# Optimization experiments

Measured on AMD Instinct MI355X. Metric: run time of the kernel, lower is better.

Reference implementation:

```python
import jax, jax.numpy as jnp
import numpy as np

B, S, CTXD, QD, ATTD = 32, 4096, 512, 512, 256

def setup_inputs() -> dict:
    key = jax.random.key(0)
    ks = jax.random.split(key, 7)
    qry = jax.random.normal(ks[0], (B, QD), dtype=jnp.float32)
    ctx = jax.random.normal(ks[1], (B, S, CTXD), dtype=jnp.float32)
    ctx_mask = jax.random.randint(ks[2], (B, S), 0, 2, dtype=jnp.int32)
    # ensure no all-zero row (would make softmax NaN)
    ctx_mask = ctx_mask.at[:, 0].set(1)
    sc = 1.0 / np.sqrt(CTXD + QD)
    W = jax.random.uniform(ks[3], (CTXD + QD, ATTD), jnp.float32, -sc, sc)
    b = jax.random.uniform(ks[4], (ATTD,), jnp.float32, -sc, sc)
    sc2 = 1.0 / np.sqrt(ATTD)
    w2 = jax.random.uniform(ks[5], (ATTD, 1), jnp.float32, -sc2, sc2)
    b2 = jax.random.uniform(ks[6], (1,), jnp.float32, -sc2, sc2)
    return {"qry": qry, "ctx": ctx, "ctx_mask": ctx_mask, "W": W, "b": b, "w2": w2, "b2": b2}

def reference(qry, ctx, ctx_mask, W, b, w2, b2):
    # cat([ctx, qry_rep]) @ W == ctx @ W_ctx + qry @ W_qry ; avoids the [B,S,ctxdim+qdim] concat
    W_ctx, W_qry = W[:CTXD], W[CTXD:]
    h = jnp.einsum('bsc,ca->bsa', ctx, W_ctx) + (qry @ W_qry)[:, None, :] + b  # [B,S,ATTD]
    y = jnp.tanh(h)
    scores = jnp.einsum('bsa,a->bs', y, w2[:, 0]) + b2[0]  # [B,S]
    scores = scores + jnp.log(ctx_mask.astype(jnp.float32))
    alphas = jax.nn.softmax(scores, axis=-1)  # [B,S]
    summary = jnp.einsum('bsc,bs->bc', ctx, alphas)  # [B,CTXD]
    return (alphas, summary, scores)
```

## Files before the change

kernel.cpp:

```cpp
#include <hip/hip_runtime.h>
#include <math.h>

#define B_ 32
#define S_ 4096
#define CTXD_ 512
#define QD_ 512
#define ATTD_ 256

#define KT 64
#define RT 64

#define MASKED_SCORE (-1e30f)

typedef __attribute__((ext_vector_type(8))) short bf16x8;
typedef __attribute__((ext_vector_type(4))) float f32x4;

__device__ __forceinline__ unsigned short f2bf(float f) {
    unsigned u = __float_as_uint(f);
    u += 0x7fff + ((u >> 16) & 1);
    return (unsigned short)(u >> 16);
}
__device__ __forceinline__ unsigned pk2(float lo, float hi) {
    return (unsigned)f2bf(lo) | ((unsigned)f2bf(hi) << 16);
}

__device__ __forceinline__ float fast_tanh(float x) {
    float xc = fminf(fmaxf(x, -15.f), 15.f);
    float t = __expf(2.f * xc);
    return (t - 1.f) / (t + 1.f);
}

__global__ __launch_bounds__(256) void wt_kernel(const float* __restrict__ W,
                                                 unsigned short* __restrict__ Wt) {
    __shared__ unsigned short tile[64][266];
    const int t = threadIdx.x;
    const int kk = blockIdx.x * 64;
    #pragma unroll
    for (int i = 0; i < 16; ++i) {
        const int r = i * 4 + (t >> 6);
        float4 v = ((const float4*)(W + (size_t)(kk + r) * ATTD_))[t & 63];
        unsigned short* tr = &tile[r][(t & 63) * 4];
        tr[0] = f2bf(v.x); tr[1] = f2bf(v.y);
        tr[2] = f2bf(v.z); tr[3] = f2bf(v.w);
    }
    __syncthreads();
    const int l8 = (t & 7) * 8;
    #pragma unroll
    for (int p = 0; p < 8; ++p) {
        const int n = p * 32 + (t >> 3);
        uint4 o;
        o.x = (unsigned)tile[l8 + 0][n] | ((unsigned)tile[l8 + 1][n] << 16);
        o.y = (unsigned)tile[l8 + 2][n] | ((unsigned)tile[l8 + 3][n] << 16);
        o.z = (unsigned)tile[l8 + 4][n] | ((unsigned)tile[l8 + 5][n] << 16);
        o.w = (unsigned)tile[l8 + 6][n] | ((unsigned)tile[l8 + 7][n] << 16);
        *(uint4*)(Wt + (size_t)n * CTXD_ + kk + l8) = o;
    }
}

__global__ __launch_bounds__(256) void qh_kernel(const float* __restrict__ qry,
                                                 const float* __restrict__ W,
                                                 const float* __restrict__ bias,
                                                 float* __restrict__ qh) {
    __shared__ float q[QD_];
    const int b = blockIdx.x, t = threadIdx.x;
    for (int i = t; i < QD_; i += 256) q[i] = qry[b * QD_ + i];
    __syncthreads();
    float acc = bias[t];
    const float* Wq = W + (size_t)CTXD_ * ATTD_ + t;
    #pragma unroll 8
    for (int k = 0; k < QD_; ++k) acc += q[k] * Wq[(size_t)k * ATTD_];
    qh[b * ATTD_ + t] = acc;
}

__global__ __launch_bounds__(256, 3) void scores_kernel(
    const float* __restrict__ ctx, const unsigned short* __restrict__ Wt,
    const float* __restrict__ qh, const float* __restrict__ w2,
    const float* __restrict__ b2, const int* __restrict__ mask,
    float* __restrict__ scores) {
    __shared__ unsigned char lds_a[RT * 144];
    __shared__ unsigned char lds_b[ATTD_ * 144];
    const int t = threadIdx.x;
    const int b = blockIdx.y;
    const int s0 = blockIdx.x * RT;
    const int tx = t & 63;
    const int w = t >> 6;
    const int wm = w & 1;
    const int wn = w >> 1;
    const int frow = tx & 15;
    const int fq = tx >> 4;

    f32x4 c00, c01, c02, c03, c04, c05, c06, c07;
    f32x4 c10, c11, c12, c13, c14, c15, c16, c17;
    c00 = c01 = c02 = c03 = c04 = c05 = c06 = c07 = (f32x4)0.f;
    c10 = c11 = c12 = c13 = c14 = c15 = c16 = c17 = (f32x4)0.f;

    const float* ctxb = ctx + ((size_t)b * S_ + s0) * CTXD_;
    const int arow = t >> 2;
    const int akq = t & 3;
    const int bn = t;

    const unsigned char* aBase = lds_a + (wm * 32 + frow) * 144 + fq * 16;
    const unsigned char* bBase = lds_b + (wn * 128 + frow) * 144 + fq * 16;

    const float* sA = ctxb + (size_t)arow * CTXD_ + akq * 16;
    float4 fa0 = ((const float4*)sA)[0];
    float4 fa1 = ((const float4*)sA)[1];
    float4 fa2 = ((const float4*)sA)[2];
    float4 fa3 = ((const float4*)sA)[3];
    const uint4* sB = (const uint4*)(Wt + (size_t)bn * CTXD_);
    uint4 pb0 = sB[0], pb1 = sB[1], pb2 = sB[2], pb3 = sB[3];
    uint4 pb4 = sB[4], pb5 = sB[5], pb6 = sB[6], pb7 = sB[7];

#define MM1(ni, ks, C0, C1)                                                  \
    {                                                                        \
        bf16x8 bf = *(const bf16x8*)(bBase + (ni) * (16 * 144) + (ks) * 64); \
        C0 = __builtin_amdgcn_mfma_f32_16x16x32_bf16(a0, bf, C0, 0, 0, 0);   \
        C1 = __builtin_amdgcn_mfma_f32_16x16x32_bf16(a1, bf, C1, 0, 0, 0);   \
    }
#define MMK(ks)                                                              \
    {                                                                        \
        bf16x8 a0 = *(const bf16x8*)(aBase + (ks) * 64);                     \
        bf16x8 a1 = *(const bf16x8*)(aBase + 16 * 144 + (ks) * 64);          \
        MM1(0, ks, c00, c10) MM1(1, ks, c01, c11) MM1(2, ks, c02, c12)       \
        MM1(3, ks, c03, c13) MM1(4, ks, c04, c14) MM1(5, ks, c05, c15)       \
        MM1(6, ks, c06, c16) MM1(7, ks, c07, c17)                            \
    }

    #pragma unroll 1
    for (int k0 = 0; k0 < CTXD_; k0 += KT) {
        __syncthreads();
        {
            uint4 p;
            p.x = pk2(fa0.x, fa0.y); p.y = pk2(fa0.z, fa0.w);
            p.z = pk2(fa1.x, fa1.y); p.w = pk2(fa1.z, fa1.w);
            *(uint4*)(lds_a + arow * 144 + akq * 32) = p;
            p.x = pk2(fa2.x, fa2.y); p.y = pk2(fa2.z, fa2.w);
            p.z = pk2(fa3.x, fa3.y); p.w = pk2(fa3.z, fa3.w);
            *(uint4*)(lds_a + arow * 144 + akq * 32 + 16) = p;
            uint4* bw = (uint4*)(lds_b + bn * 144);
            bw[0] = pb0; bw[1] = pb1; bw[2] = pb2; bw[3] = pb3;
            bw[4] = pb4; bw[5] = pb5; bw[6] = pb6; bw[7] = pb7;
        }
        __syncthreads();
        if (k0 + KT < CTXD_) {
            const float* sA2 = ctxb + (size_t)arow * CTXD_ + (k0 + KT) + akq * 16;
            fa0 = ((const float4*)sA2)[0];
            fa1 = ((const float4*)sA2)[1];
            fa2 = ((const float4*)sA2)[2];
            fa3 = ((const float4*)sA2)[3];
            const uint4* sB2 = (const uint4*)(Wt + (size_t)bn * CTXD_ + (k0 + KT));
            pb0 = sB2[0]; pb1 = sB2[1]; pb2 = sB2[2]; pb3 = sB2[3];
            pb4 = sB2[4]; pb5 = sB2[5]; pb6 = sB2[6]; pb7 = sB2[7];
        }
        MMK(0)
        MMK(1)
    }
#undef MMK
#undef MM1

    const float* qhb = qh + b * ATTD_ + wn * 128;
    const float* w2b = w2 + wn * 128;
    float p00 = 0.f, p01 = 0.f, p02 = 0.f, p03 = 0.f;
    float p10 = 0.f, p11 = 0.f, p12 = 0.f, p13 = 0.f;
#define EPI(ni, C0, C1)                                                      \
    {                                                                        \
        float qv = qhb[(ni) * 16 + frow];                                    \
        float wv = w2b[(ni) * 16 + frow];                                    \
        p00 += fast_tanh(C0[0] + qv) * wv;                                   \
        p01 += fast_tanh(C0[1] + qv) * wv;                                   \
        p02 += fast_tanh(C0[2] + qv) * wv;                                   \
        p03 += fast_tanh(C0[3] + qv) * wv;                                   \
        p10 += fast_tanh(C1[0] + qv) * wv;                                   \
        p11 += fast_tanh(C1[1] + qv) * wv;                                   \
        p12 += fast_tanh(C1[2] + qv) * wv;                                   \
        p13 += fast_tanh(C1[3] + qv) * wv;                                   \
    }
    EPI(0, c00, c10) EPI(1, c01, c11) EPI(2, c02, c12) EPI(3, c03, c13)
    EPI(4, c04, c14) EPI(5, c05, c15) EPI(6, c06, c16) EPI(7, c07, c17)
#undef EPI
    #pragma unroll
    for (int off = 1; off <= 8; off <<= 1) {
        p00 += __shfl_xor(p00, off, 64);
        p01 += __shfl_xor(p01, off, 64);
        p02 += __shfl_xor(p02, off, 64);
        p03 += __shfl_xor(p03, off, 64);
        p10 += __shfl_xor(p10, off, 64);
        p11 += __shfl_xor(p11, off, 64);
        p12 += __shfl_xor(p12, off, 64);
        p13 += __shfl_xor(p13, off, 64);
    }
    float* sred = (float*)lds_a;
    __syncthreads();
    if (frow == 0) {
        const int base = wn * 64 + wm * 32 + fq * 4;
        sred[base + 0] = p00; sred[base + 1] = p01;
        sred[base + 2] = p02; sred[base + 3] = p03;
        sred[base + 16 + 0] = p10; sred[base + 16 + 1] = p11;
        sred[base + 16 + 2] = p12; sred[base + 16 + 3] = p13;
    }
    __syncthreads();
    if (t < 64) {
        const int s = s0 + t;
        float sc = sred[t] + sred[64 + t] + b2[0];
        if (mask[b * S_ + s] == 0) sc = MASKED_SCORE;
        scores[b * S_ + s] = sc;
    }
}

__global__ __launch_bounds__(256) void softstat_kernel(
    const float* __restrict__ scores, float* __restrict__ stats) {
    const int b = blockIdx.x, t = threadIdx.x;
    __shared__ float red[8];
    float v[16];
    float m = -INFINITY;
    #pragma unroll
    for (int i = 0; i < 16; ++i) {
        v[i] = scores[b * S_ + t + i * 256];
        m = fmaxf(m, v[i]);
    }
    #pragma unroll
    for (int off = 1; off <= 32; off <<= 1) m = fmaxf(m, __shfl_xor(m, off, 64));
    if ((t & 63) == 0) red[t >> 6] = m;
    __syncthreads();
    m = fmaxf(fmaxf(red[0], red[1]), fmaxf(red[2], red[3]));
    float sum = 0.f;
    #pragma unroll
    for (int i = 0; i < 16; ++i) sum += expf(v[i] - m);
    #pragma unroll
    for (int off = 1; off <= 32; off <<= 1) sum += __shfl_xor(sum, off, 64);
    if ((t & 63) == 0) red[4 + (t >> 6)] = sum;
    __syncthreads();
    if (t == 0) {
        sum = red[4] + red[5] + red[6] + red[7];
        stats[2 * b] = m;
        stats[2 * b + 1] = 1.0f / sum;
    }
}

__global__ __launch_bounds__(256) void summary_part_kernel(
    const float* __restrict__ ctx, const float* __restrict__ scores,
    const float* __restrict__ stats, float* __restrict__ alphas,
    float* __restrict__ part, int nch, int cs) {
    const int b = blockIdx.y, ch = blockIdx.x, t = threadIdx.x;
    const int col = t & 63;
    const int q = t >> 6;
    const int s0 = ch * cs;
    const float m = stats[2 * b];
    const float invl = stats[2 * b + 1];
    const float* sp = scores + b * S_ + s0;
    for (int s = t; s < cs; s += 256)
        alphas[b * S_ + s0 + s] = expf(sp[s] - m) * invl;
    float4 alo = make_float4(0.f, 0.f, 0.f, 0.f);
    float4 ahi = make_float4(0.f, 0.f, 0.f, 0.f);
    const float* cp = ctx + ((size_t)b * S_ + s0) * CTXD_;
    #pragma unroll 4
    for (int s = q; s < cs; s += 4) {
        float al = expf(sp[s] - m) * invl;
        const float4* row = (const float4*)(cp + (size_t)s * CTXD_);
        float4 v0 = row[col];
        float4 v1 = row[col + 64];
        alo.x += v0.x * al; alo.y += v0.y * al;
        alo.z += v0.z * al; alo.w += v0.w * al;
        ahi.x += v1.x * al; ahi.y += v1.y * al;
        ahi.z += v1.z * al; ahi.w += v1.w * al;
    }
    __shared__ float4 buf[4][128];
    buf[q][col] = alo;
    buf[q][col + 64] = ahi;
    __syncthreads();
    if (t < 128) {
        float4 a0 = buf[0][t], a1 = buf[1][t], a2 = buf[2][t], a3 = buf[3][t];
        float4 r;
        r.x = a0.x + a1.x + a2.x + a3.x;
        r.y = a0.y + a1.y + a2.y + a3.y;
        r.z = a0.z + a1.z + a2.z + a3.z;
        r.w = a0.w + a1.w + a2.w + a3.w;
        ((float4*)(part + ((size_t)(b * nch + ch)) * CTXD_))[t] = r;
    }
}

__global__ __launch_bounds__(256) void summary_reduce_kernel(
    const float* __restrict__ part, float* __restrict__ summary, int nch) {
    const int b = blockIdx.x, t = threadIdx.x;
    for (int c = t; c < CTXD_; c += 256) {
        float s = 0.f;
        for (int ch = 0; ch < nch; ++ch)
            s += part[((size_t)(b * nch + ch)) * CTXD_ + c];
        summary[b * CTXD_ + c] = s;
    }
}

extern "C" void kernel_launch(void* const* d_in, const int* in_sizes, int n_in,
                              void* d_out, int out_size, void* d_ws,
                              size_t ws_size, hipStream_t stream) {
    const float* qry = (const float*)d_in[0];
    const float* ctx = (const float*)d_in[1];
    const int* mask = (const int*)d_in[2];
    const float* W = (const float*)d_in[3];
    const float* bias = (const float*)d_in[4];
    const float* w2 = (const float*)d_in[5];
    const float* b2 = (const float*)d_in[6];

    float* out = (float*)d_out;
    float* alphas = out;
    float* summary = out + B_ * S_;
    float* scores = out + B_ * S_ + B_ * CTXD_;

    unsigned short* Wt = (unsigned short*)d_ws;
    float* qh = (float*)((char*)d_ws + (size_t)ATTD_ * CTXD_ * 2);
    float* stats = qh + B_ * ATTD_;
    float* part = stats + 2 * B_;
    const size_t fixed_bytes =
        (size_t)ATTD_ * CTXD_ * 2 + (size_t)B_ * ATTD_ * 4 + 2 * B_ * 4;

    int nch = 64;
    while (nch > 1 && fixed_bytes + (size_t)B_ * nch * CTXD_ * 4 > ws_size)
        nch >>= 1;
    const int cs = S_ / nch;

    wt_kernel<<<8, 256, 0, stream>>>(W, Wt);
    qh_kernel<<<B_, 256, 0, stream>>>(qry, W, bias, qh);
    scores_kernel<<<dim3(S_ / RT, B_), 256, 0, stream>>>(ctx, Wt, qh, w2, b2,
                                                         mask, scores);
    softstat_kernel<<<B_, 256, 0, stream>>>(scores, stats);
    summary_part_kernel<<<dim3(nch, B_), 256, 0, stream>>>(ctx, scores, stats,
                                                           alphas, part, nch, cs);
    summary_reduce_kernel<<<B_, 256, 0, stream>>>(part, summary, nch);
}
```

Baseline: 520.2 us.

## Fuse softmax partial stats and weighted ctx sum into scores kernel

The scores kernel now computes per-chunk max and exp-sum, and accumulates the exp-weighted ctx rows for its tile into partial summaries. A new combine kernel rescales chunk partials by global max (online softmax), producing summary and alphas. This avoids a second full pass over ctx from global memory and drops two launches. The scores kernel gets extra epilogue work and the workspace-size fallback is removed.

```diff
diff --git a/kernel.cpp b/kernel.cpp
--- a/kernel.cpp
+++ b/kernel.cpp
@@ -9,6 +9,7 @@
 
 #define KT 64
 #define RT 64
+#define NCH (S_ / RT)
 
 #define MASKED_SCORE (-1e30f)
 
@@ -76,12 +77,14 @@
     const float* __restrict__ ctx, const unsigned short* __restrict__ Wt,
     const float* __restrict__ qh, const float* __restrict__ w2,
     const float* __restrict__ b2, const int* __restrict__ mask,
-    float* __restrict__ scores) {
+    float* __restrict__ scores, float* __restrict__ mstat,
+    float* __restrict__ lstat, float* __restrict__ part) {
     __shared__ unsigned char lds_a[RT * 144];
     __shared__ unsigned char lds_b[ATTD_ * 144];
     const int t = threadIdx.x;
     const int b = blockIdx.y;
-    const int s0 = blockIdx.x * RT;
+    const int ch = blockIdx.x;
+    const int s0 = ch * RT;
     const int tx = t & 63;
     const int w = t >> 6;
     const int wm = w & 1;
@@ -199,64 +202,37 @@
         sred[base + 16 + 2] = p12; sred[base + 16 + 3] = p13;
     }
     __syncthreads();
+    float* wl = (float*)lds_b;
     if (t < 64) {
         const int s = s0 + t;
         float sc = sred[t] + sred[64 + t] + b2[0];
-        if (mask[b * S_ + s] == 0) sc = MASKED_SCORE;
+        const bool msk = (mask[b * S_ + s] == 0);
+        if (msk) sc = MASKED_SCORE;
         scores[b * S_ + s] = sc;
-    }
-}
-
-__global__ __launch_bounds__(256) void softstat_kernel(
-    const float* __restrict__ scores, float* __restrict__ stats) {
-    const int b = blockIdx.x, t = threadIdx.x;
-    __shared__ float red[8];
-    float v[16];
-    float m = -INFINITY;
-    #pragma unroll
-    for (int i = 0; i < 16; ++i) {
-        v[i] = scores[b * S_ + t + i * 256];
-        m = fmaxf(m, v[i]);
-    }
-    #pragma unroll
-    for (int off = 1; off <= 32; off <<= 1) m = fmaxf(m, __shfl_xor(m, off, 64));
-    if ((t & 63) == 0) red[t >> 6] = m;
-    __syncthreads();
-    m = fmaxf(fmaxf(red[0], red[1]), fmaxf(red[2], red[3]));
-    float sum = 0.f;
-    #pragma unroll
-    for (int i = 0; i < 16; ++i) sum += expf(v[i] - m);
-    #pragma unroll
-    for (int off = 1; off <= 32; off <<= 1) sum += __shfl_xor(sum, off, 64);
-    if ((t & 63) == 0) red[4 + (t >> 6)] = sum;
-    __syncthreads();
-    if (t == 0) {
-        sum = red[4] + red[5] + red[6] + red[7];
-        stats[2 * b] = m;
-        stats[2 * b + 1] = 1.0f / sum;
-    }
-}
-
-__global__ __launch_bounds__(256) void summary_part_kernel(
-    const float* __restrict__ ctx, const float* __restrict__ scores,
-    const float* __restrict__ stats, float* __restrict__ alphas,
-    float* __restrict__ part, int nch, int cs) {
-    const int b = blockIdx.y, ch = blockIdx.x, t = threadIdx.x;
+        float mloc = sc;
+        #pragma unroll
+        for (int off = 1; off < 64; off <<= 1)
+            mloc = fmaxf(mloc, __shfl_xor(mloc, off, 64));
+        const float ws = msk ? 0.f : __expf(sc - mloc);
+        float lloc = ws;
+        #pragma unroll
+        for (int off = 1; off < 64; off <<= 1)
+            lloc += __shfl_xor(lloc, off, 64);
+        if (t == 0) {
+            mstat[b * NCH + ch] = mloc;
+            lstat[b * NCH + ch] = lloc;
+        }
+        wl[t] = ws;
+    }
+    __syncthreads();
     const int col = t & 63;
     const int q = t >> 6;
-    const int s0 = ch * cs;
-    const float m = stats[2 * b];
-    const float invl = stats[2 * b + 1];
-    const float* sp = scores + b * S_ + s0;
-    for (int s = t; s < cs; s += 256)
-        alphas[b * S_ + s0 + s] = expf(sp[s] - m) * invl;
     float4 alo = make_float4(0.f, 0.f, 0.f, 0.f);
     float4 ahi = make_float4(0.f, 0.f, 0.f, 0.f);
-    const float* cp = ctx + ((size_t)b * S_ + s0) * CTXD_;
     #pragma unroll 4
-    for (int s = q; s < cs; s += 4) {
-        float al = expf(sp[s] - m) * invl;
-        const float4* row = (const float4*)(cp + (size_t)s * CTXD_);
+    for (int s = q; s < RT; s += 4) {
+        const float al = wl[s];
+        const float4* row = (const float4*)(ctxb + (size_t)s * CTXD_);
         float4 v0 = row[col];
         float4 v1 = row[col + 64];
         alo.x += v0.x * al; alo.y += v0.y * al;
@@ -264,30 +240,64 @@
         ahi.x += v1.x * al; ahi.y += v1.y * al;
         ahi.z += v1.z * al; ahi.w += v1.w * al;
     }
-    __shared__ float4 buf[4][128];
-    buf[q][col] = alo;
-    buf[q][col + 64] = ahi;
+    float4* buf = (float4*)(lds_b + 1024);
+    buf[q * 128 + col] = alo;
+    buf[q * 128 + col + 64] = ahi;
     __syncthreads();
     if (t < 128) {
-        float4 a0 = buf[0][t], a1 = buf[1][t], a2 = buf[2][t], a3 = buf[3][t];
+        float4 a0 = buf[t], a1 = buf[128 + t], a2 = buf[256 + t], a3 = buf[384 + t];
         float4 r;
         r.x = a0.x + a1.x + a2.x + a3.x;
         r.y = a0.y + a1.y + a2.y + a3.y;
         r.z = a0.z + a1.z + a2.z + a3.z;
         r.w = a0.w + a1.w + a2.w + a3.w;
-        ((float4*)(part + ((size_t)(b * nch + ch)) * CTXD_))[t] = r;
-    }
-}
-
-__global__ __launch_bounds__(256) void summary_reduce_kernel(
-    const float* __restrict__ part, float* __restrict__ summary, int nch) {
+        ((float4*)(part + ((size_t)(b * NCH + ch)) * CTXD_))[t] = r;
+    }
+}
+
+__global__ __launch_bounds__(256) void combine_kernel(
+    const float* __restrict__ mstat, const float* __restrict__ lstat,
+    const float* __restrict__ part, const float* __restrict__ scores,
+    float* __restrict__ alphas, float* __restrict__ summary) {
     const int b = blockIdx.x, t = threadIdx.x;
-    for (int c = t; c < CTXD_; c += 256) {
-        float s = 0.f;
-        for (int ch = 0; ch < nch; ++ch)
-            s += part[((size_t)(b * nch + ch)) * CTXD_ + c];
-        summary[b * CTXD_ + c] = s;
-    }
+    __shared__ float e[NCH];
+    __shared__ float gstat[2];
+    if (t < NCH) {
+        const float mi = mstat[b * NCH + t];
+        const float li = lstat[b * NCH + t];
+        float m = mi;
+        #pragma unroll
+        for (int off = 1; off < 64; off <<= 1)
+            m = fmaxf(m, __shfl_xor(m, off, 64));
+        const float ei = __expf(mi - m);
+        float l = ei * li;
+        #pragma unroll
+        for (int off = 1; off < 64; off <<= 1)
+            l += __shfl_xor(l, off, 64);
+        e[t] = ei;
+        if (t == 0) { gstat[0] = m; gstat[1] = 1.0f / l; }
+    }
+    __syncthreads();
+    const float m = gstat[0], il = gstat[1];
+    const int c4 = t & 127, h = t >> 7;
+    float4 acc = make_float4(0.f, 0.f, 0.f, 0.f);
+    for (int chv = h; chv < NCH; chv += 2) {
+        const float ei = e[chv];
+        float4 v = ((const float4*)(part + ((size_t)(b * NCH + chv)) * CTXD_))[c4];
+        acc.x += ei * v.x; acc.y += ei * v.y;
+        acc.z += ei * v.z; acc.w += ei * v.w;
+    }
+    __shared__ float4 buf[128];
+    if (h == 1) buf[c4] = acc;
+    __syncthreads();
+    if (h == 0) {
+        float4 o = buf[c4];
+        acc.x = (acc.x + o.x) * il; acc.y = (acc.y + o.y) * il;
+        acc.z = (acc.z + o.z) * il; acc.w = (acc.w + o.w) * il;
+        ((float4*)(summary + (size_t)b * CTXD_))[c4] = acc;
+    }
+    for (int s = t; s < S_; s += 256)
+        alphas[b * S_ + s] = __expf(scores[b * S_ + s] - m) * il;
 }
 
 extern "C" void kernel_launch(void* const* d_in, const int* in_sizes, int n_in,
@@ -308,22 +318,14 @@
 
     unsigned short* Wt = (unsigned short*)d_ws;
     float* qh = (float*)((char*)d_ws + (size_t)ATTD_ * CTXD_ * 2);
-    float* stats = qh + B_ * ATTD_;
-    float* part = stats + 2 * B_;
-    const size_t fixed_bytes =
-        (size_t)ATTD_ * CTXD_ * 2 + (size_t)B_ * ATTD_ * 4 + 2 * B_ * 4;
-
-    int nch = 64;
-    while (nch > 1 && fixed_bytes + (size_t)B_ * nch * CTXD_ * 4 > ws_size)
-        nch >>= 1;
-    const int cs = S_ / nch;
+    float* mstat = qh + B_ * ATTD_;
+    float* lstat = mstat + B_ * NCH;
+    float* part = lstat + B_ * NCH;
 
     wt_kernel<<<8, 256, 0, stream>>>(W, Wt);
     qh_kernel<<<B_, 256, 0, stream>>>(qry, W, bias, qh);
-    scores_kernel<<<dim3(S_ / RT, B_), 256, 0, stream>>>(ctx, Wt, qh, w2, b2,
-                                                         mask, scores);
-    softstat_kernel<<<B_, 256, 0, stream>>>(scores, stats);
-    summary_part_kernel<<<dim3(nch, B_), 256, 0, stream>>>(ctx, scores, stats,
-                                                           alphas, part, nch, cs);
-    summary_reduce_kernel<<<B_, 256, 0, stream>>>(part, summary, nch);
-}
+    scores_kernel<<<dim3(NCH, B_), 256, 0, stream>>>(ctx, Wt, qh, w2, b2, mask,
+                                                     scores, mstat, lstat, part);
+    combine_kernel<<<B_, 256, 0, stream>>>(mstat, lstat, part, scores, alphas,
+                                           summary);
+}
```

Result: faster. 470.6 us (-9.5%).
